# Kernel tuning notes

Hardware: AMD Instinct MI355X
Metric: run time of the kernel (lower is better)

## Reference

```python
import jax, jax.numpy as jnp
import numpy as np

BATCH, L, OUT, DIM, VOCAB, K = 25, 11, 4, 2048, 32000, 1024


def setup_inputs() -> dict:
    key = jax.random.key(0)
    k1, k2, k3 = jax.random.split(key, 3)
    h = jax.random.normal(k1, (BATCH, L, OUT, DIM), dtype=jnp.float32)
    lm_head_weight = jax.random.normal(k2, (VOCAB, DIM), dtype=jnp.float32) * 0.02
    index = jax.random.randint(k3, (BATCH, L, K), 0, VOCAB, dtype=jnp.int64)
    return {"h": h, "lm_head_weight": lm_head_weight, "index": index}


def reference(h, lm_head_weight, index):
    # Faithful to torch: full-vocab matmul h @ weight.T, then gather selected ids.
    # h: (b, l, o, d); weight: (v, d) -> logits: (b, l, o, v)
    logits = jnp.einsum('blod,vd->blov', h, lm_head_weight)
    # gather along vocab dim with index (b, l, k) expanded over the o axis
    b, l, o, v = logits.shape
    idx = jnp.broadcast_to(index[:, :, None, :], (b, l, o, index.shape[-1]))
    result = jnp.take_along_axis(logits, idx, axis=3)  # (b, l, o, k)
    return result
```

## Files before the change

### kernel.cpp

```cpp
#include <hip/hip_runtime.h>

#define BATCH 25
#define LSEQ  11
#define OUTR  4
#define DIM   2048
#define VOCAB 32000
#define KSEL  1024

#define KPB   64
#define KPW   16

__global__ __launch_bounds__(256) void ehead_kernel(
    const float* __restrict__ h,
    const float* __restrict__ wt,
    const int*   __restrict__ index,
    float*       __restrict__ out)
{
    const int nkc = KSEL / KPB;
    const int bl  = blockIdx.x / nkc;
    const int kc  = blockIdx.x % nkc;
    const int kbase = kc * KPB;

    __shared__ float hs[OUTR * DIM];

    const float* hp = h + (size_t)bl * (OUTR * DIM);
    const int tid = threadIdx.x;

#pragma unroll
    for (int i = 0; i < (OUTR * DIM) / (256 * 4); ++i) {
        const int e = (i * 256 + tid) * 4;
        *(float4*)&hs[e] = *(const float4*)&hp[e];
    }
    __syncthreads();

    const int wave = tid >> 6;
    const int lane = tid & 63;

    const int*  ip = index + (size_t)bl * KSEL + kbase + wave * KPW;
    float*      op = out   + (size_t)bl * (OUTR * KSEL) + kbase + wave * KPW;

    for (int g = 0; g < KPW; g += 4) {
        const int i0 = ip[g + 0];
        const int i1 = ip[g + 1];
        const int i2 = ip[g + 2];
        const int i3 = ip[g + 3];
        const float4* r0 = (const float4*)(wt + (size_t)i0 * DIM);
        const float4* r1 = (const float4*)(wt + (size_t)i1 * DIM);
        const float4* r2 = (const float4*)(wt + (size_t)i2 * DIM);
        const float4* r3 = (const float4*)(wt + (size_t)i3 * DIM);

        float acc[OUTR][4];
#pragma unroll
        for (int o = 0; o < OUTR; ++o)
#pragma unroll
            for (int kk = 0; kk < 4; ++kk) acc[o][kk] = 0.f;

#pragma unroll
        for (int c = 0; c < DIM / 256; ++c) {
            const int off = c * 64 + lane;
            const float4 w0 = r0[off];
            const float4 w1 = r1[off];
            const float4 w2 = r2[off];
            const float4 w3 = r3[off];
#pragma unroll
            for (int o = 0; o < OUTR; ++o) {
                const float4 hv = *(const float4*)&hs[o * DIM + off * 4];
                acc[o][0] += hv.x * w0.x + hv.y * w0.y + hv.z * w0.z + hv.w * w0.w;
                acc[o][1] += hv.x * w1.x + hv.y * w1.y + hv.z * w1.z + hv.w * w1.w;
                acc[o][2] += hv.x * w2.x + hv.y * w2.y + hv.z * w2.z + hv.w * w2.w;
                acc[o][3] += hv.x * w3.x + hv.y * w3.y + hv.z * w3.z + hv.w * w3.w;
            }
        }

#pragma unroll
        for (int o = 0; o < OUTR; ++o)
#pragma unroll
            for (int kk = 0; kk < 4; ++kk) {
                float v = acc[o][kk];
#pragma unroll
                for (int s = 32; s >= 1; s >>= 1) v += __shfl_xor(v, s, 64);
                acc[o][kk] = v;
            }

        if (lane < 16) {
            float v = 0.f;
#pragma unroll
            for (int oo = 0; oo < OUTR; ++oo)
#pragma unroll
                for (int qq = 0; qq < 4; ++qq)
                    v = (oo * 4 + qq == lane) ? acc[oo][qq] : v;
            const int o  = lane >> 2;
            const int kk = lane & 3;
            op[o * KSEL + g + kk] = v;
        }
    }
}

extern "C" void kernel_launch(void* const* d_in, const int* in_sizes, int n_in,
                              void* d_out, int out_size, void* d_ws, size_t ws_size,
                              hipStream_t stream) {
    const float* h   = (const float*)d_in[0];
    const float* wt  = (const float*)d_in[1];
    const int*   idx = (const int*)d_in[2];
    float*       out = (float*)d_out;

    const int grid = BATCH * LSEQ * (KSEL / KPB);
    ehead_kernel<<<grid, 256, 0, stream>>>(h, wt, idx, out);
}
```

Before: 604.2 us.

## Convert LM head weights to bf16 in workspace before the gathered dot products

Adds a pre-pass kernel that converts the full fp32 weight matrix to bf16 in the workspace, with round-to-nearest-even. A new gather kernel then reads the selected bf16 rows, which halves the bytes fetched per gathered row. It keeps h in registers instead of shared memory and doubles the number of indices handled per block. The cost is an extra full pass over the weights on every call, plus lower-precision weights that may move results closer to the tolerance limit. The old fp32 path is kept as a fallback when the workspace is too small.

```diff
diff --git a/kernel.cpp b/kernel.cpp
--- a/kernel.cpp
+++ b/kernel.cpp
@@ -7,25 +7,128 @@
 #define VOCAB 32000
 #define KSEL  1024
 
-#define KPB   64
-#define KPW   16
-
-__global__ __launch_bounds__(256) void ehead_kernel(
+#define KPB   128
+#define KPW   32
+#define NKC   (KSEL / KPB)
+#define WBF_BYTES ((size_t)VOCAB * DIM * 2)
+
+__global__ __launch_bounds__(256) void conv_kernel(const float* __restrict__ w,
+                                                   ushort* __restrict__ wbf) {
+    const size_t i = ((size_t)blockIdx.x * 256 + threadIdx.x) * 8;
+    const float4 a = *(const float4*)(w + i);
+    const float4 b = *(const float4*)(w + i + 4);
+    uint4 o;
+    auto cvt2 = [](float lo, float hi) -> unsigned int {
+        unsigned int ul = __float_as_uint(lo), uh = __float_as_uint(hi);
+        ul = (ul + 0x7FFFu + ((ul >> 16) & 1u)) >> 16;
+        uh = (uh + 0x7FFFu + ((uh >> 16) & 1u)) >> 16;
+        return ul | (uh << 16);
+    };
+    o.x = cvt2(a.x, a.y); o.y = cvt2(a.z, a.w);
+    o.z = cvt2(b.x, b.y); o.w = cvt2(b.z, b.w);
+    *(uint4*)(wbf + i) = o;
+}
+
+__global__ __launch_bounds__(256, 2) void gather_bf16_kernel(
+    const float*  __restrict__ h,
+    const ushort* __restrict__ wbf,
+    const int*    __restrict__ index,
+    float*        __restrict__ out)
+{
+    const int bl    = blockIdx.x / NKC;
+    const int kc    = blockIdx.x % NKC;
+    const int kbase = kc * KPB;
+    const int tid   = threadIdx.x;
+    const int wave  = tid >> 6;
+    const int lane  = tid & 63;
+
+    float4 hreg[OUTR][4][2];
+    const float* hp = h + (size_t)bl * (OUTR * DIM);
+#pragma unroll
+    for (int o = 0; o < OUTR; ++o)
+#pragma unroll
+        for (int c = 0; c < 4; ++c) {
+            const float* p = hp + o * DIM + c * 512 + lane * 8;
+            hreg[o][c][0] = *(const float4*)p;
+            hreg[o][c][1] = *(const float4*)(p + 4);
+        }
+
+    const int* ip = index + (size_t)bl * KSEL + kbase + wave * KPW;
+    float*     op = out   + (size_t)bl * (OUTR * KSEL) + kbase + wave * KPW;
+
+    for (int g = 0; g < KPW; g += 4) {
+        uint4 wv[4][4];
+#pragma unroll
+        for (int r = 0; r < 4; ++r) {
+            const uint4* rp = (const uint4*)(wbf + (size_t)ip[g + r] * DIM);
+#pragma unroll
+            for (int c = 0; c < 4; ++c) wv[r][c] = rp[c * 64 + lane];
+        }
+
+        float acc[OUTR][4];
+#pragma unroll
+        for (int o = 0; o < OUTR; ++o)
+#pragma unroll
+            for (int r = 0; r < 4; ++r) acc[o][r] = 0.f;
+
+#pragma unroll
+        for (int r = 0; r < 4; ++r)
+#pragma unroll
+            for (int c = 0; c < 4; ++c) {
+                const unsigned int* wd = (const unsigned int*)&wv[r][c];
+#pragma unroll
+                for (int m = 0; m < 4; ++m) {
+                    const float flo = __uint_as_float(wd[m] << 16);
+                    const float fhi = __uint_as_float(wd[m] & 0xFFFF0000u);
+#pragma unroll
+                    for (int o = 0; o < OUTR; ++o) {
+                        const float* hh = (const float*)&hreg[o][c][0];
+                        acc[o][r] += flo * hh[2 * m] + fhi * hh[2 * m + 1];
+                    }
+                }
+            }
+
+#pragma unroll
+        for (int o = 0; o < OUTR; ++o)
+#pragma unroll
+            for (int r = 0; r < 4; ++r) {
+                float v = acc[o][r];
+#pragma unroll
+                for (int s = 32; s >= 1; s >>= 1) v += __shfl_xor(v, s, 64);
+                acc[o][r] = v;
+            }
+
+        if (lane < 16) {
+            float v = 0.f;
+#pragma unroll
+            for (int oo = 0; oo < OUTR; ++oo)
+#pragma unroll
+                for (int rr = 0; rr < 4; ++rr)
+                    v = (oo * 4 + rr == lane) ? acc[oo][rr] : v;
+            const int o = lane >> 2;
+            const int r = lane & 3;
+            op[o * KSEL + g + r] = v;
+        }
+    }
+}
+
+#define FKPB 64
+#define FKPW 16
+
+__global__ __launch_bounds__(256) void ehead_f32_kernel(
     const float* __restrict__ h,
     const float* __restrict__ wt,
     const int*   __restrict__ index,
     float*       __restrict__ out)
 {
-    const int nkc = KSEL / KPB;
+    const int nkc = KSEL / FKPB;
     const int bl  = blockIdx.x / nkc;
     const int kc  = blockIdx.x % nkc;
-    const int kbase = kc * KPB;
+    const int kbase = kc * FKPB;
 
     __shared__ float hs[OUTR * DIM];
-
     const float* hp = h + (size_t)bl * (OUTR * DIM);
     const int tid = threadIdx.x;
-
 #pragma unroll
     for (int i = 0; i < (OUTR * DIM) / (256 * 4); ++i) {
         const int e = (i * 256 + tid) * 4;
@@ -35,26 +138,19 @@
 
     const int wave = tid >> 6;
     const int lane = tid & 63;
-
-    const int*  ip = index + (size_t)bl * KSEL + kbase + wave * KPW;
-    float*      op = out   + (size_t)bl * (OUTR * KSEL) + kbase + wave * KPW;
-
-    for (int g = 0; g < KPW; g += 4) {
-        const int i0 = ip[g + 0];
-        const int i1 = ip[g + 1];
-        const int i2 = ip[g + 2];
-        const int i3 = ip[g + 3];
-        const float4* r0 = (const float4*)(wt + (size_t)i0 * DIM);
-        const float4* r1 = (const float4*)(wt + (size_t)i1 * DIM);
-        const float4* r2 = (const float4*)(wt + (size_t)i2 * DIM);
-        const float4* r3 = (const float4*)(wt + (size_t)i3 * DIM);
-
+    const int* ip = index + (size_t)bl * KSEL + kbase + wave * FKPW;
+    float*     op = out   + (size_t)bl * (OUTR * KSEL) + kbase + wave * FKPW;
+
+    for (int g = 0; g < FKPW; g += 4) {
+        const float4* r0 = (const float4*)(wt + (size_t)ip[g + 0] * DIM);
+        const float4* r1 = (const float4*)(wt + (size_t)ip[g + 1] * DIM);
+        const float4* r2 = (const float4*)(wt + (size_t)ip[g + 2] * DIM);
+        const float4* r3 = (const float4*)(wt + (size_t)ip[g + 3] * DIM);
         float acc[OUTR][4];
 #pragma unroll
         for (int o = 0; o < OUTR; ++o)
 #pragma unroll
             for (int kk = 0; kk < 4; ++kk) acc[o][kk] = 0.f;
-
 #pragma unroll
         for (int c = 0; c < DIM / 256; ++c) {
             const int off = c * 64 + lane;
@@ -71,7 +167,6 @@
                 acc[o][3] += hv.x * w3.x + hv.y * w3.y + hv.z * w3.z + hv.w * w3.w;
             }
         }
-
 #pragma unroll
         for (int o = 0; o < OUTR; ++o)
 #pragma unroll
@@ -81,7 +176,6 @@
                 for (int s = 32; s >= 1; s >>= 1) v += __shfl_xor(v, s, 64);
                 acc[o][kk] = v;
             }
-
         if (lane < 16) {
             float v = 0.f;
 #pragma unroll
@@ -89,9 +183,7 @@
 #pragma unroll
                 for (int qq = 0; qq < 4; ++qq)
                     v = (oo * 4 + qq == lane) ? acc[oo][qq] : v;
-            const int o  = lane >> 2;
-            const int kk = lane & 3;
-            op[o * KSEL + g + kk] = v;
+            op[(lane >> 2) * KSEL + g + (lane & 3)] = v;
         }
     }
 }
@@ -104,6 +196,13 @@
     const int*   idx = (const int*)d_in[2];
     float*       out = (float*)d_out;
 
-    const int grid = BATCH * LSEQ * (KSEL / KPB);
-    ehead_kernel<<<grid, 256, 0, stream>>>(h, wt, idx, out);
-}
+    if (ws_size >= WBF_BYTES) {
+        ushort* wbf = (ushort*)d_ws;
+        conv_kernel<<<(VOCAB * DIM) / (256 * 8), 256, 0, stream>>>(wt, wbf);
+        const int grid = BATCH * LSEQ * NKC;
+        gather_bf16_kernel<<<grid, 256, 0, stream>>>(h, wbf, idx, out);
+    } else {
+        const int grid = BATCH * LSEQ * (KSEL / FKPB);
+        ehead_f32_kernel<<<grid, 256, 0, stream>>>(h, wt, idx, out);
+    }
+}
```

New measurement: 551.1 us. 8.8% less time.

## Convert weights to fp16 and compute gathered dot products with MFMA

Applied to the files above, without the earlier changes.

Adds a pre-pass kernel that converts the full fp32 lm_head weight to fp16 in workspace, then a gather kernel that uses 16x16x32 fp16 MFMA instructions on gathered rows against fp16 h held in shared memory. The aim is to halve the bytes read in the gather phase and move the arithmetic from scalar FMAs plus shuffle reductions onto matrix cores. The conversion reads and writes the entire 32000x2048 weight on every call, far more than the rows actually gathered, and fp16 rounding reduces accuracy. The old fp32 kernel stays as a fallback when the workspace is too small.

```diff
diff --git a/kernel.cpp b/kernel.cpp
--- a/kernel.cpp
+++ b/kernel.cpp
@@ -7,54 +7,139 @@
 #define VOCAB 32000
 #define KSEL  1024
 
-#define KPB   64
-#define KPW   16
+typedef _Float16 half8  __attribute__((ext_vector_type(8)));
+typedef float    floatx4 __attribute__((ext_vector_type(4)));
 
-__global__ __launch_bounds__(256) void ehead_kernel(
+#define WH_BYTES ((size_t)VOCAB * DIM * 2)
+
+__global__ __launch_bounds__(256) void conv_f16(const float* __restrict__ w,
+                                                _Float16* __restrict__ wh) {
+    const size_t i = ((size_t)blockIdx.x * 256 + threadIdx.x) * 8;
+    const floatx4 a = __builtin_nontemporal_load((const floatx4*)(w + i));
+    const floatx4 b = __builtin_nontemporal_load((const floatx4*)(w + i + 4));
+    half8 hv;
+    hv[0] = (_Float16)a[0]; hv[1] = (_Float16)a[1];
+    hv[2] = (_Float16)a[2]; hv[3] = (_Float16)a[3];
+    hv[4] = (_Float16)b[0]; hv[5] = (_Float16)b[1];
+    hv[6] = (_Float16)b[2]; hv[7] = (_Float16)b[3];
+    *(half8*)(wh + i) = hv;
+}
+
+#define TPW 4
+#define KPB (4 * TPW * 16)
+#define NKC (KSEL / KPB)
+#define ROWE 2080
+
+__global__ __launch_bounds__(256) void gather_mfma(
+    const float*    __restrict__ h,
+    const _Float16* __restrict__ wh,
+    const int*      __restrict__ index,
+    float*          __restrict__ out)
+{
+    __shared__ _Float16 hs[OUTR * ROWE];
+
+    const int bl   = blockIdx.x / NKC;
+    const int kc   = blockIdx.x % NKC;
+    const int tid  = threadIdx.x;
+    const int wave = tid >> 6;
+    const int lane = tid & 63;
+    const int quad = lane >> 4;
+    const int n    = lane & 15;
+    const int row  = lane & 3;
+
+    const float* hp = h + (size_t)bl * (OUTR * DIM);
+#pragma unroll
+    for (int o = 0; o < OUTR; ++o) {
+        const int e = o * DIM + tid * 8;
+        const floatx4 a = *(const floatx4*)(hp + e);
+        const floatx4 b = *(const floatx4*)(hp + e + 4);
+        half8 hv;
+        hv[0] = (_Float16)a[0]; hv[1] = (_Float16)a[1];
+        hv[2] = (_Float16)a[2]; hv[3] = (_Float16)a[3];
+        hv[4] = (_Float16)b[0]; hv[5] = (_Float16)b[1];
+        hv[6] = (_Float16)b[2]; hv[7] = (_Float16)b[3];
+        *(half8*)(hs + o * ROWE + tid * 8) = hv;
+    }
+    __syncthreads();
+
+    const int kb_blk = kc * KPB;
+    const _Float16* bptr[TPW];
+#pragma unroll
+    for (int t = 0; t < TPW; ++t) {
+        const int k_id = kb_blk + (wave * TPW + t) * 16 + n;
+        const int ridx = index[(size_t)bl * KSEL + k_id];
+        bptr[t] = wh + (size_t)ridx * DIM + quad * 8;
+    }
+
+    const _Float16* aptr = hs + row * ROWE + quad * 8;
+
+    floatx4 acc[TPW];
+#pragma unroll
+    for (int t = 0; t < TPW; ++t) acc[t] = (floatx4){0.f, 0.f, 0.f, 0.f};
+
+#pragma unroll 4
+    for (int ks = 0; ks < DIM / 32; ++ks) {
+        const half8 a = *(const half8*)(aptr + ks * 32);
+        half8 b[TPW];
+#pragma unroll
+        for (int t = 0; t < TPW; ++t)
+            b[t] = *(const half8*)(bptr[t] + ks * 32);
+#pragma unroll
+        for (int t = 0; t < TPW; ++t)
+            acc[t] = __builtin_amdgcn_mfma_f32_16x16x32_f16(a, b[t], acc[t], 0, 0, 0);
+    }
+
+    if (quad == 0) {
+        float* op = out + (size_t)bl * (OUTR * KSEL) + kb_blk;
+#pragma unroll
+        for (int t = 0; t < TPW; ++t) {
+            const int kcol = (wave * TPW + t) * 16 + n;
+#pragma unroll
+            for (int r = 0; r < OUTR; ++r)
+                op[r * KSEL + kcol] = acc[t][r];
+        }
+    }
+}
+
+#define FKPB 64
+#define FKPW 16
+
+__global__ __launch_bounds__(256) void ehead_f32_kernel(
     const float* __restrict__ h,
     const float* __restrict__ wt,
     const int*   __restrict__ index,
     float*       __restrict__ out)
 {
-    const int nkc = KSEL / KPB;
+    const int nkc = KSEL / FKPB;
     const int bl  = blockIdx.x / nkc;
     const int kc  = blockIdx.x % nkc;
-    const int kbase = kc * KPB;
+    const int kbase = kc * FKPB;
 
-    __shared__ float hs[OUTR * DIM];
-
+    __shared__ float hsf[OUTR * DIM];
     const float* hp = h + (size_t)bl * (OUTR * DIM);
     const int tid = threadIdx.x;
-
 #pragma unroll
     for (int i = 0; i < (OUTR * DIM) / (256 * 4); ++i) {
         const int e = (i * 256 + tid) * 4;
-        *(float4*)&hs[e] = *(const float4*)&hp[e];
+        *(float4*)&hsf[e] = *(const float4*)&hp[e];
     }
     __syncthreads();
 
     const int wave = tid >> 6;
     const int lane = tid & 63;
+    const int* ip = index + (size_t)bl * KSEL + kbase + wave * FKPW;
+    float*     op = out   + (size_t)bl * (OUTR * KSEL) + kbase + wave * FKPW;
 
-    const int*  ip = index + (size_t)bl * KSEL + kbase + wave * KPW;
-    float*      op = out   + (size_t)bl * (OUTR * KSEL) + kbase + wave * KPW;
-
-    for (int g = 0; g < KPW; g += 4) {
-        const int i0 = ip[g + 0];
-        const int i1 = ip[g + 1];
-        const int i2 = ip[g + 2];
-        const int i3 = ip[g + 3];
-        const float4* r0 = (const float4*)(wt + (size_t)i0 * DIM);
-        const float4* r1 = (const float4*)(wt + (size_t)i1 * DIM);
-        const float4* r2 = (const float4*)(wt + (size_t)i2 * DIM);
-        const float4* r3 = (const float4*)(wt + (size_t)i3 * DIM);
-
+    for (int g = 0; g < FKPW; g += 4) {
+        const float4* r0 = (const float4*)(wt + (size_t)ip[g + 0] * DIM);
+        const float4* r1 = (const float4*)(wt + (size_t)ip[g + 1] * DIM);
+        const float4* r2 = (const float4*)(wt + (size_t)ip[g + 2] * DIM);
+        const float4* r3 = (const float4*)(wt + (size_t)ip[g + 3] * DIM);
         float acc[OUTR][4];
 #pragma unroll
         for (int o = 0; o < OUTR; ++o)
 #pragma unroll
             for (int kk = 0; kk < 4; ++kk) acc[o][kk] = 0.f;
-
 #pragma unroll
         for (int c = 0; c < DIM / 256; ++c) {
             const int off = c * 64 + lane;
@@ -64,14 +149,13 @@
             const float4 w3 = r3[off];
 #pragma unroll
             for (int o = 0; o < OUTR; ++o) {
-                const float4 hv = *(const float4*)&hs[o * DIM + off * 4];
+                const float4 hv = *(const float4*)&hsf[o * DIM + off * 4];
                 acc[o][0] += hv.x * w0.x + hv.y * w0.y + hv.z * w0.z + hv.w * w0.w;
                 acc[o][1] += hv.x * w1.x + hv.y * w1.y + hv.z * w1.z + hv.w * w1.w;
                 acc[o][2] += hv.x * w2.x + hv.y * w2.y + hv.z * w2.z + hv.w * w2.w;
                 acc[o][3] += hv.x * w3.x + hv.y * w3.y + hv.z * w3.z + hv.w * w3.w;
             }
         }
-
 #pragma unroll
         for (int o = 0; o < OUTR; ++o)
 #pragma unroll
@@ -81,7 +165,6 @@
                 for (int s = 32; s >= 1; s >>= 1) v += __shfl_xor(v, s, 64);
                 acc[o][kk] = v;
             }
-
         if (lane < 16) {
             float v = 0.f;
 #pragma unroll
@@ -89,9 +172,7 @@
 #pragma unroll
                 for (int qq = 0; qq < 4; ++qq)
                     v = (oo * 4 + qq == lane) ? acc[oo][qq] : v;
-            const int o  = lane >> 2;
-            const int kk = lane & 3;
-            op[o * KSEL + g + kk] = v;
+            op[(lane >> 2) * KSEL + g + (lane & 3)] = v;
         }
     }
 }
@@ -104,6 +185,13 @@
     const int*   idx = (const int*)d_in[2];
     float*       out = (float*)d_out;
 
-    const int grid = BATCH * LSEQ * (KSEL / KPB);
-    ehead_kernel<<<grid, 256, 0, stream>>>(h, wt, idx, out);
+    if (ws_size >= WH_BYTES) {
+        _Float16* wh = (_Float16*)d_ws;
+        conv_f16<<<(VOCAB * DIM) / (256 * 8), 256, 0, stream>>>(wt, wh);
+        const int grid = BATCH * LSEQ * NKC;
+        gather_mfma<<<grid, 256, 0, stream>>>(h, wh, idx, out);
+    } else {
+        const int grid = BATCH * LSEQ * (KSEL / FKPB);
+        ehead_f32_kernel<<<grid, 256, 0, stream>>>(h, wt, idx, out);
+    }
 }
```

Result: faster. 518.4 us (-14.2%).
